# Kernel optimization log

Hardware: AMD Instinct MI355X
Metric: run time of the kernel (lower is better)

## Reference

```python
import jax, jax.numpy as jnp
import numpy as np

N_NODES = 500_000
N_EDGES = 8_000_000
NUM_GRAPHS = 512


def _glorot(key, shape):
    lim = float(np.sqrt(6.0 / (shape[0] + shape[1])))
    return jax.random.uniform(key, shape, jnp.float32, -lim, lim)


def setup_inputs() -> dict:
    key = jax.random.key(0)
    ks = jax.random.split(key, 10)
    x = jax.random.normal(ks[0], (N_NODES, 3), jnp.float32)
    edge_index = jax.random.randint(ks[1], (2, N_EDGES), 0, N_NODES, jnp.int64)
    batch = jnp.sort(jax.random.randint(ks[2], (N_NODES,), 0, NUM_GRAPHS, jnp.int64))
    return {
        "x": x,
        "edge_index": edge_index,
        "batch": batch,
        # GCNConv weights stored [in, out]; bias [out]
        "W1": _glorot(ks[3], (3, 16)),
        "b1": jnp.zeros((16,), jnp.float32),
        "W2": _glorot(ks[4], (16, 32)),
        "b2": jnp.zeros((32,), jnp.float32),
        "fW1": _glorot(ks[5], (32, 64)),
        "fb1": jnp.zeros((64,), jnp.float32),
        "fW2": _glorot(ks[6], (64, 3)),
        "fb2": jnp.zeros((3,), jnp.float32),
    }


def _gcn_conv(x, edge_index, W, b):
    n = x.shape[0]
    src, dst = edge_index[0], edge_index[1]
    h = x @ W  # [N, out]
    ones = jnp.ones((edge_index.shape[1],), h.dtype)
    deg = jax.ops.segment_sum(ones, dst, num_segments=n) + 1.0  # in-degree + self loop
    dinv = jax.lax.rsqrt(deg)
    norm = dinv[src] * dinv[dst]  # [E]
    agg = jax.ops.segment_sum(norm[:, None] * h[src], dst, num_segments=n)
    # self-loop contribution: norm_ii = dinv_i^2
    return agg + (dinv * dinv)[:, None] * h + b


def reference(x, edge_index, batch, W1, b1, W2, b2, fW1, fb1, fW2, fb2):
    h = jax.nn.relu(_gcn_conv(x, edge_index, W1, b1))
    h = jax.nn.relu(_gcn_conv(h, edge_index, W2, b2))
    # global_mean_pool over graph ids
    sums = jax.ops.segment_sum(h, batch, num_segments=NUM_GRAPHS)
    cnts = jax.ops.segment_sum(jnp.ones((h.shape[0],), h.dtype), batch, num_segments=NUM_GRAPHS)
    pooled = sums / jnp.maximum(cnts, 1.0)[:, None]  # [G, 32]
    z = jax.nn.relu(pooled @ fW1 + fb1)
    z = z @ fW2 + fb2
    return jax.nn.log_softmax(z, axis=1)
```

## Files before the change

kernel.cpp:

```cpp
#include <hip/hip_runtime.h>
#include <hip/hip_bf16.h>

constexpr int N_NODES    = 500000;
constexpr int N_EDGES    = 8000000;
constexpr int NUM_GRAPHS = 512;

constexpr int BSHIFT = 11;
constexpr int BSIZE  = 1 << BSHIFT;
constexpr int NBKT   = (N_NODES + BSIZE - 1) / BSIZE;
constexpr int EPB    = 4096;
constexpr int NBLK_A = (N_EDGES + EPB - 1) / EPB;
constexpr int NH     = NBKT * NBLK_A;
constexpr int SCAN_B = 256;
constexpr int NSB    = (NH + SCAN_B - 1) / SCAN_B;
constexpr int TSH    = 16;
constexpr int CAP    = 20480;

__device__ __forceinline__ float bf_lo(unsigned u) { return __uint_as_float(u << 16); }
__device__ __forceinline__ float bf_hi(unsigned u) { return __uint_as_float(u & 0xFFFF0000u); }
__device__ __forceinline__ unsigned short f2bf(float f) {
  unsigned u = __float_as_uint(f);
  return (unsigned short)((u + 0x7FFFu + ((u >> 16) & 1u)) >> 16);
}
__device__ __forceinline__ unsigned packbf(float a, float b) {
  return (unsigned)f2bf(a) | ((unsigned)f2bf(b) << 16);
}

__device__ __forceinline__ unsigned f2e4m3(float x) {
  x = fminf(x, 448.0f);
  unsigned xb = __float_as_uint(x);
  int e = (int)(xb >> 23) - 127;
  if (e < -6) {
    int m = (int)rintf(x * 512.0f);
    return (m <= 7) ? (unsigned)m : 0x08u;
  }
  unsigned lsb = (xb >> 20) & 1;
  unsigned r = xb + 0x7FFFFu + lsb;
  int e2 = (int)(r >> 23) - 127;
  unsigned m3 = (r >> 20) & 7;
  return (unsigned)(((e2 + 7) << 3) | m3);
}
__device__ __forceinline__ float e4m3f(unsigned b) {
  unsigned e = (b >> 3) & 0xF, m = b & 7;
  float norm = __uint_as_float(((e + 120u) << 23) | (m << 20));
  float den = (float)m * 0.001953125f;
  return e ? norm : den;
}

__global__ void k_hist(const int* __restrict__ dst, int* __restrict__ H) {
  __shared__ int h[NBKT];
  for (int i = threadIdx.x; i < NBKT; i += blockDim.x) h[i] = 0;
  __syncthreads();
  int e0 = blockIdx.x * EPB;
  int e1 = min(e0 + EPB, N_EDGES);
  for (int e = e0 + threadIdx.x; e < e1; e += blockDim.x)
    atomicAdd(&h[dst[e] >> BSHIFT], 1);
  __syncthreads();
  for (int i = threadIdx.x; i < NBKT; i += blockDim.x)
    H[i * NBLK_A + blockIdx.x] = h[i];
}

__global__ void k_scan1(const int* __restrict__ in, int* __restrict__ out,
                        int* __restrict__ bsum, int n) {
  __shared__ int tmp[SCAN_B];
  int t = threadIdx.x;
  int i = blockIdx.x * SCAN_B + t;
  int v = (i < n) ? in[i] : 0;
  tmp[t] = v;
  __syncthreads();
  for (int off = 1; off < SCAN_B; off <<= 1) {
    int a = (t >= off) ? tmp[t - off] : 0;
    __syncthreads();
    tmp[t] += a;
    __syncthreads();
  }
  if (i < n) out[i] = tmp[t] - v;
  if (t == SCAN_B - 1) bsum[blockIdx.x] = tmp[t];
}

__global__ void k_scan2(int* __restrict__ bsum, int nb) {
  __shared__ int tmp[SCAN_B];
  int t = threadIdx.x;
  int carry = 0;
  for (int base = 0; base < nb; base += SCAN_B) {
    int i = base + t;
    int v = (i < nb) ? bsum[i] : 0;
    tmp[t] = v;
    __syncthreads();
    for (int off = 1; off < SCAN_B; off <<= 1) {
      int a = (t >= off) ? tmp[t - off] : 0;
      __syncthreads();
      tmp[t] += a;
      __syncthreads();
    }
    if (i < nb) bsum[i] = carry + tmp[t] - v;
    carry += tmp[SCAN_B - 1];
    __syncthreads();
  }
}

__device__ __forceinline__ int s_at(const int* Sarr, const int* bsum, int idx) {
  return Sarr[idx] + bsum[idx >> 8];
}

__global__ void k_scatter_bkt(const int* __restrict__ src, const int* __restrict__ dst,
                              const int* __restrict__ Sarr, const int* __restrict__ bsum,
                              int* __restrict__ pairs) {
  __shared__ int lcnt[256];
  __shared__ int lofs[256];
  __shared__ int base[256];
  __shared__ int pout[EPB];
  __shared__ unsigned char bout[EPB];
  int t = threadIdx.x;
  int blk = blockIdx.x;
  int e0 = blk * EPB;
  int e1 = min(e0 + EPB, N_EDGES);
  int ne = e1 - e0;
  lcnt[t] = 0;
  __syncthreads();
  for (int e = e0 + t; e < e1; e += 256)
    atomicAdd(&lcnt[dst[e] >> BSHIFT], 1);
  __syncthreads();
  lofs[t] = lcnt[t];
  __syncthreads();
  for (int off = 1; off < 256; off <<= 1) {
    int v = (t >= off) ? lofs[t - off] : 0;
    __syncthreads();
    lofs[t] += v;
    __syncthreads();
  }
  lofs[t] -= lcnt[t];
  base[t] = (t < NBKT) ? s_at(Sarr, bsum, t * NBLK_A + blk) : 0;
  lcnt[t] = 0;
  __syncthreads();
  for (int e = e0 + t; e < e1; e += 256) {
    int d = dst[e], s = src[e];
    int b = d >> BSHIFT;
    int r = atomicAdd(&lcnt[b], 1);
    int q = lofs[b] + r;
    pout[q] = ((d & (BSIZE - 1)) << 19) | s;
    bout[q] = (unsigned char)b;
  }
  __syncthreads();
  for (int li = t; li < ne; li += 256) {
    int b = bout[li];
    pairs[base[b] + (li - lofs[b])] = pout[li];
  }
}

__global__ void __launch_bounds__(1024)
k_csr(const int* __restrict__ pairs, const int* __restrict__ Sarr,
      const int* __restrict__ bsum, const float* __restrict__ x,
      int* __restrict__ ssrc, int* __restrict__ offs,
      float* __restrict__ dinv, unsigned* __restrict__ xsb) {
  __shared__ int hist[8192];
  __shared__ int sout[CAP];
  __shared__ int tmp[1024];
  int t = threadIdx.x;
  int bkt = blockIdx.x >> 1;
  int h = blockIdx.x & 1;
  int e0 = s_at(Sarr, bsum, bkt * NBLK_A);
  int e1 = (bkt + 1 < NBKT) ? s_at(Sarr, bsum, (bkt + 1) * NBLK_A) : N_EDGES;
#pragma unroll
  for (int j = 0; j < 8; ++j) hist[t + (j << 10)] = 0;
  __syncthreads();
  int lc = 0;
  for (int e = e0 + t; e < e1; e += 1024) {
    int p = pairs[e];
    int nl = p >> 19;
    int s = p & 0x7FFFF;
    if ((nl >> 10) == h) atomicAdd(&hist[((s >> TSH) << 10) | (nl & 1023)], 1);
    else if ((nl >> 10) == 0) lc++;
  }
  tmp[t] = lc;
  __syncthreads();
  for (int off = 512; off > 0; off >>= 1) {
    if (t < off) tmp[t] += tmp[t + off];
    __syncthreads();
  }
  int halfbase = h ? tmp[0] : 0;
  __syncthreads();
  int c[8];
  int tsum = 0;
#pragma unroll
  for (int j = 0; j < 8; ++j) { c[j] = hist[(j << 10) | t]; tsum += c[j]; }
  tmp[t] = tsum;
  __syncthreads();
  for (int off = 1; off < 1024; off <<= 1) {
    int a = (t >= off) ? tmp[t - off] : 0;
    __syncthreads();
    tmp[t] += a;
    __syncthreads();
  }
  int run = tmp[t] - tsum;
  int total = tmp[1023];
  {
    int b = run;
#pragma unroll
    for (int j = 0; j < 8; ++j) { int cc = c[j]; hist[(j << 10) | t] = b; b += cc; }
  }
  int n = (bkt << BSHIFT) + (h << 10) + t;
  if (n < N_NODES) {
    offs[n] = e0 + halfbase + run;
    float di = rsqrtf((float)tsum + 1.0f);
    dinv[n] = di;
    const float* xs = x + (size_t)n * 3;
    uint2 v = make_uint2(packbf(di * xs[0], di * xs[1]), packbf(di * xs[2], 0.0f));
    *(uint2*)(xsb + (size_t)n * 2) = v;
  }
  __syncthreads();
  int base = e0 + halfbase;
  if (total <= CAP) {
    for (int e = e0 + t; e < e1; e += 1024) {
      int p = pairs[e];
      int nl = p >> 19;
      if ((nl >> 10) != h) continue;
      int s = p & 0x7FFFF;
      int r = atomicAdd(&hist[((s >> TSH) << 10) | (nl & 1023)], 1);
      sout[r] = s;
    }
    __syncthreads();
    for (int q = t; q < total; q += 1024)
      ssrc[base + q] = sout[q];
  } else {
    for (int e = e0 + t; e < e1; e += 1024) {
      int p = pairs[e];
      int nl = p >> 19;
      if ((nl >> 10) != h) continue;
      int s = p & 0x7FFFF;
      int r = atomicAdd(&hist[((s >> TSH) << 10) | (nl & 1023)], 1);
      ssrc[base + r] = s;
    }
  }
  if (bkt == 0 && h == 0 && t == 0) offs[N_NODES] = N_EDGES;
}

__global__ void k_g1f1(const int* __restrict__ ssrc, const int* __restrict__ offs,
                       const unsigned* __restrict__ xsb, const float* __restrict__ dinv,
                       const float* __restrict__ W1, const float* __restrict__ b1,
                       unsigned* __restrict__ ub) {
  unsigned t = blockIdx.x * blockDim.x + threadIdx.x;
  unsigned n = t >> 1;
  int j = t & 1;
  if (n >= (unsigned)N_NODES) return;
  int o0 = offs[n], o1 = offs[n + 1];
  float a0 = 0.0f, a1 = 0.0f;
  int i = o0;
  for (; i + 1 < o1; i += 2) {
    int s0 = ssrc[i], s1 = ssrc[i + 1];
    unsigned q0 = xsb[(size_t)s0 * 2 + j];
    unsigned q1 = xsb[(size_t)s1 * 2 + j];
    a0 += bf_lo(q0) + bf_lo(q1);
    a1 += bf_hi(q0) + bf_hi(q1);
  }
  if (i < o1) {
    unsigned q = xsb[(size_t)ssrc[i] * 2 + j];
    a0 += bf_lo(q); a1 += bf_hi(q);
  }
  float oth0 = __shfl_xor(a0, 1);
  float oth1 = __shfl_xor(a1, 1);
  float A0 = j ? oth0 : a0;
  float A1v = j ? oth1 : a1;
  float A2v = j ? a0 : oth0;
  float di = dinv[n];
  uint2 xq = *(const uint2*)&xsb[(size_t)n * 2];
  float t0 = di * (A0 + bf_lo(xq.x));
  float t1 = di * (A1v + bf_hi(xq.x));
  float t2 = di * (A2v + bf_lo(xq.y));
  unsigned w0 = 0, w1 = 0;
#pragma unroll
  for (int q8 = 0; q8 < 4; ++q8) {
    int f = 8 * j + 2 * q8;
    float v0 = t0 * W1[f]     + t1 * W1[16 + f]     + t2 * W1[32 + f]     + b1[f];
    float v1 = t0 * W1[f + 1] + t1 * W1[16 + f + 1] + t2 * W1[32 + f + 1] + b1[f + 1];
    unsigned pb = f2e4m3(di * fmaxf(v0, 0.0f)) | (f2e4m3(di * fmaxf(v1, 0.0f)) << 8);
    if (q8 < 2) w0 |= pb << (16 * q8); else w1 |= pb << (16 * (q8 - 2));
  }
  *(uint2*)&ub[(size_t)n * 4 + j * 2] = make_uint2(w0, w1);
}

__global__ void k_gather2(const int* __restrict__ ssrc, const int* __restrict__ offs,
                          const unsigned* __restrict__ ub, float* __restrict__ A2) {
  __shared__ float lut[128];
  if (threadIdx.x < 128) lut[threadIdx.x] = e4m3f(threadIdx.x);
  __syncthreads();
  unsigned t = blockIdx.x * blockDim.x + threadIdx.x;
  unsigned n = t >> 2;
  int j = t & 3;
  if (n >= (unsigned)N_NODES) return;
  int o0 = offs[n], o1 = offs[n + 1];
  unsigned qs = ub[(size_t)n * 4 + j];
  float a0 = lut[qs & 0x7F];
  float a1 = lut[(qs >> 8) & 0x7F];
  float a2 = lut[(qs >> 16) & 0x7F];
  float a3 = lut[(qs >> 24) & 0x7F];
  int i = o0;
  for (; i + 1 < o1; i += 2) {
    int s0 = ssrc[i], s1 = ssrc[i + 1];
    unsigned q0 = ub[(size_t)s0 * 4 + j];
    unsigned q1 = ub[(size_t)s1 * 4 + j];
    a0 += lut[q0 & 0x7F]         + lut[q1 & 0x7F];
    a1 += lut[(q0 >> 8) & 0x7F]  + lut[(q1 >> 8) & 0x7F];
    a2 += lut[(q0 >> 16) & 0x7F] + lut[(q1 >> 16) & 0x7F];
    a3 += lut[(q0 >> 24) & 0x7F] + lut[(q1 >> 24) & 0x7F];
  }
  if (i < o1) {
    unsigned q = ub[(size_t)ssrc[i] * 4 + j];
    a0 += lut[q & 0x7F];
    a1 += lut[(q >> 8) & 0x7F];
    a2 += lut[(q >> 16) & 0x7F];
    a3 += lut[(q >> 24) & 0x7F];
  }
  *(float4*)&A2[(size_t)n * 16 + j * 4] = make_float4(a0, a1, a2, a3);
}

__global__ void k_pool2(const float* __restrict__ A2,
                        const float* __restrict__ W2, const float* __restrict__ b2,
                        const float* __restrict__ dinv, const int* __restrict__ batch,
                        float* __restrict__ sums) {
  int f = threadIdx.x & 31, sub = threadIdx.x >> 5;
  int n0 = blockIdx.x * 128 + sub * 16;
  int n1 = min(n0 + 16, N_NODES);
  if (n0 >= n1) return;
  float w2col[16];
#pragma unroll
  for (int k = 0; k < 16; ++k) w2col[k] = W2[k * 32 + f];
  float bf = b2[f];
  int cur = batch[n0];
  float acc = 0.0f;
  for (int n = n0; n < n1; ++n) {
    int g = batch[n];
    if (g != cur) { atomicAdd(&sums[(size_t)cur * 32 + f], acc); acc = 0.0f; cur = g; }
    const float4* a2p = (const float4*)(A2 + (size_t)n * 16);
    float4 aa0 = a2p[0], aa1 = a2p[1], aa2 = a2p[2], aa3 = a2p[3];
    float v = aa0.x * w2col[0]  + aa0.y * w2col[1]  + aa0.z * w2col[2]  + aa0.w * w2col[3]
            + aa1.x * w2col[4]  + aa1.y * w2col[5]  + aa1.z * w2col[6]  + aa1.w * w2col[7]
            + aa2.x * w2col[8]  + aa2.y * w2col[9]  + aa2.z * w2col[10] + aa2.w * w2col[11]
            + aa3.x * w2col[12] + aa3.y * w2col[13] + aa3.z * w2col[14] + aa3.w * w2col[15];
    v = dinv[n] * v + bf;
    acc += fmaxf(v, 0.0f);
  }
  atomicAdd(&sums[(size_t)cur * 32 + f], acc);
}

__global__ void k_mlp(const float* __restrict__ sums, const int* __restrict__ batch,
                      const float* __restrict__ fW1, const float* __restrict__ fb1,
                      const float* __restrict__ fW2, const float* __restrict__ fb2,
                      float* __restrict__ out) {
  __shared__ float w1s[32 * 64];
  __shared__ float w2s[64 * 3];
  __shared__ float b1s[64];
  __shared__ float b2s[3];
  for (int i = threadIdx.x; i < 32 * 64; i += blockDim.x) w1s[i] = fW1[i];
  for (int i = threadIdx.x; i < 64 * 3; i += blockDim.x) w2s[i] = fW2[i];
  for (int i = threadIdx.x; i < 64; i += blockDim.x) b1s[i] = fb1[i];
  for (int i = threadIdx.x; i < 3; i += blockDim.x) b2s[i] = fb2[i];
  __syncthreads();
  int g = blockIdx.x * blockDim.x + threadIdx.x;
  if (g >= NUM_GRAPHS) return;
  int lo = 0, hi = N_NODES;
  while (lo < hi) { int mid = (lo + hi) >> 1; if (batch[mid] < g) lo = mid + 1; else hi = mid; }
  int s0 = lo;
  int lo2 = s0, hi2 = N_NODES;
  while (lo2 < hi2) { int mid = (lo2 + hi2) >> 1; if (batch[mid] < g + 1) lo2 = mid + 1; else hi2 = mid; }
  float c = fmaxf((float)(lo2 - s0), 1.0f);
  float p[32];
#pragma unroll
  for (int i = 0; i < 32; ++i) p[i] = sums[(size_t)g * 32 + i] / c;
  float z2[3] = {b2s[0], b2s[1], b2s[2]};
  for (int j = 0; j < 64; ++j) {
    float a = b1s[j];
#pragma unroll
    for (int i = 0; i < 32; ++i) a += p[i] * w1s[i * 64 + j];
    a = fmaxf(a, 0.0f);
#pragma unroll
    for (int k = 0; k < 3; ++k) z2[k] += a * w2s[j * 3 + k];
  }
  float m = fmaxf(fmaxf(z2[0], z2[1]), z2[2]);
  float l = logf(expf(z2[0] - m) + expf(z2[1] - m) + expf(z2[2] - m));
#pragma unroll
  for (int k = 0; k < 3; ++k) out[(size_t)g * 3 + k] = z2[k] - m - l;
}

extern "C" void kernel_launch(void* const* d_in, const int* in_sizes, int n_in,
                              void* d_out, int out_size, void* d_ws, size_t ws_size,
                              hipStream_t stream) {
  const float* x     = (const float*)d_in[0];
  const int*   ei    = (const int*)d_in[1];
  const int*   batch = (const int*)d_in[2];
  const float* W1    = (const float*)d_in[3];
  const float* b1    = (const float*)d_in[4];
  const float* W2    = (const float*)d_in[5];
  const float* b2    = (const float*)d_in[6];
  const float* fW1   = (const float*)d_in[7];
  const float* fb1   = (const float*)d_in[8];
  const float* fW2   = (const float*)d_in[9];
  const float* fb2   = (const float*)d_in[10];
  const int* src = ei;
  const int* dst = ei + N_EDGES;

  float* ws       = (float*)d_ws;
  float* dinv     = ws;
  unsigned* xsb   = (unsigned*)(dinv + 524288);
  unsigned* ub    = xsb + 1048576;
  float* scratch  = (float*)(ub + 4194304);
  float* sums     = scratch + 2000000;
  int* offs       = (int*)(sums + 16384);
  int* ssrc       = offs + 524288;
  int* pairs      = ssrc + 8000000;
  int* H    = (int*)scratch;
  int* Sarr = H + 478730;
  int* bsum = Sarr + 478730;
  float* A2 = (float*)pairs;

  hipMemsetAsync(sums, 0, (size_t)NUM_GRAPHS * 32 * 4, stream);

  const int B = 256;
  k_hist<<<NBLK_A, B, 0, stream>>>(dst, H);
  k_scan1<<<NSB, SCAN_B, 0, stream>>>(H, Sarr, bsum, NH);
  k_scan2<<<1, SCAN_B, 0, stream>>>(bsum, NSB);
  k_scatter_bkt<<<NBLK_A, B, 0, stream>>>(src, dst, Sarr, bsum, pairs);
  k_csr<<<NBKT * 2, 1024, 0, stream>>>(pairs, Sarr, bsum, x, ssrc, offs, dinv, xsb);
  k_g1f1<<<((size_t)N_NODES * 2 + B - 1) / B, B, 0, stream>>>(ssrc, offs, xsb, dinv, W1, b1, ub);
  k_gather2<<<((size_t)N_NODES * 4 + B - 1) / B, B, 0, stream>>>(ssrc, offs, ub, A2);
  k_pool2<<<(N_NODES + 127) / 128, B, 0, stream>>>(A2, W2, b2, dinv, batch, sums);
  k_mlp<<<(NUM_GRAPHS + B - 1) / B, B, 0, stream>>>(sums, batch, fW1, fb1, fW2, fb2, (float*)d_out);
}
```

Baseline: 365.0 us.

## Split layer-2 gather into two feature halves for smaller working set

```diff
diff --git a/kernel.cpp b/kernel.cpp
--- a/kernel.cpp
+++ b/kernel.cpp
@@ -238,7 +238,7 @@
 __global__ void k_g1f1(const int* __restrict__ ssrc, const int* __restrict__ offs,
                        const unsigned* __restrict__ xsb, const float* __restrict__ dinv,
                        const float* __restrict__ W1, const float* __restrict__ b1,
-                       unsigned* __restrict__ ub) {
+                       unsigned* __restrict__ ub0, unsigned* __restrict__ ub1) {
   unsigned t = blockIdx.x * blockDim.x + threadIdx.x;
   unsigned n = t >> 1;
   int j = t & 1;
@@ -276,20 +276,21 @@
     unsigned pb = f2e4m3(di * fmaxf(v0, 0.0f)) | (f2e4m3(di * fmaxf(v1, 0.0f)) << 8);
     if (q8 < 2) w0 |= pb << (16 * q8); else w1 |= pb << (16 * (q8 - 2));
   }
-  *(uint2*)&ub[(size_t)n * 4 + j * 2] = make_uint2(w0, w1);
-}
-
-__global__ void k_gather2(const int* __restrict__ ssrc, const int* __restrict__ offs,
-                          const unsigned* __restrict__ ub, float* __restrict__ A2) {
+  unsigned* ubt = j ? ub1 : ub0;
+  *(uint2*)&ubt[(size_t)n * 2] = make_uint2(w0, w1);
+}
+
+__global__ void k_gather2h(const int* __restrict__ ssrc, const int* __restrict__ offs,
+                           const unsigned* __restrict__ ubt, float* __restrict__ A2h) {
   __shared__ float lut[128];
   if (threadIdx.x < 128) lut[threadIdx.x] = e4m3f(threadIdx.x);
   __syncthreads();
   unsigned t = blockIdx.x * blockDim.x + threadIdx.x;
-  unsigned n = t >> 2;
-  int j = t & 3;
+  unsigned n = t >> 1;
+  int j = t & 1;
   if (n >= (unsigned)N_NODES) return;
   int o0 = offs[n], o1 = offs[n + 1];
-  unsigned qs = ub[(size_t)n * 4 + j];
+  unsigned qs = ubt[(size_t)n * 2 + j];
   float a0 = lut[qs & 0x7F];
   float a1 = lut[(qs >> 8) & 0x7F];
   float a2 = lut[(qs >> 16) & 0x7F];
@@ -297,24 +298,24 @@
   int i = o0;
   for (; i + 1 < o1; i += 2) {
     int s0 = ssrc[i], s1 = ssrc[i + 1];
-    unsigned q0 = ub[(size_t)s0 * 4 + j];
-    unsigned q1 = ub[(size_t)s1 * 4 + j];
+    unsigned q0 = ubt[(size_t)s0 * 2 + j];
+    unsigned q1 = ubt[(size_t)s1 * 2 + j];
     a0 += lut[q0 & 0x7F]         + lut[q1 & 0x7F];
     a1 += lut[(q0 >> 8) & 0x7F]  + lut[(q1 >> 8) & 0x7F];
     a2 += lut[(q0 >> 16) & 0x7F] + lut[(q1 >> 16) & 0x7F];
     a3 += lut[(q0 >> 24) & 0x7F] + lut[(q1 >> 24) & 0x7F];
   }
   if (i < o1) {
-    unsigned q = ub[(size_t)ssrc[i] * 4 + j];
+    unsigned q = ubt[(size_t)ssrc[i] * 2 + j];
     a0 += lut[q & 0x7F];
     a1 += lut[(q >> 8) & 0x7F];
     a2 += lut[(q >> 16) & 0x7F];
     a3 += lut[(q >> 24) & 0x7F];
   }
-  *(float4*)&A2[(size_t)n * 16 + j * 4] = make_float4(a0, a1, a2, a3);
-}
-
-__global__ void k_pool2(const float* __restrict__ A2,
+  *(float4*)&A2h[(size_t)n * 8 + j * 4] = make_float4(a0, a1, a2, a3);
+}
+
+__global__ void k_pool2(const float* __restrict__ A2a, const float* __restrict__ A2b,
                         const float* __restrict__ W2, const float* __restrict__ b2,
                         const float* __restrict__ dinv, const int* __restrict__ batch,
                         float* __restrict__ sums) {
@@ -331,8 +332,9 @@
   for (int n = n0; n < n1; ++n) {
     int g = batch[n];
     if (g != cur) { atomicAdd(&sums[(size_t)cur * 32 + f], acc); acc = 0.0f; cur = g; }
-    const float4* a2p = (const float4*)(A2 + (size_t)n * 16);
-    float4 aa0 = a2p[0], aa1 = a2p[1], aa2 = a2p[2], aa3 = a2p[3];
+    const float4* pa = (const float4*)(A2a + (size_t)n * 8);
+    const float4* pb = (const float4*)(A2b + (size_t)n * 8);
+    float4 aa0 = pa[0], aa1 = pa[1], aa2 = pb[0], aa3 = pb[1];
     float v = aa0.x * w2col[0]  + aa0.y * w2col[1]  + aa0.z * w2col[2]  + aa0.w * w2col[3]
             + aa1.x * w2col[4]  + aa1.y * w2col[5]  + aa1.z * w2col[6]  + aa1.w * w2col[7]
             + aa2.x * w2col[8]  + aa2.y * w2col[9]  + aa2.z * w2col[10] + aa2.w * w2col[11]
@@ -402,8 +404,9 @@
   float* ws       = (float*)d_ws;
   float* dinv     = ws;
   unsigned* xsb   = (unsigned*)(dinv + 524288);
-  unsigned* ub    = xsb + 1048576;
-  float* scratch  = (float*)(ub + 4194304);
+  unsigned* ub0   = xsb + 1048576;
+  unsigned* ub1   = ub0 + 1048576;
+  float* scratch  = (float*)(xsb + 1048576 + 4194304);
   float* sums     = scratch + 2000000;
   int* offs       = (int*)(sums + 16384);
   int* ssrc       = offs + 524288;
@@ -411,7 +414,8 @@
   int* H    = (int*)scratch;
   int* Sarr = H + 478730;
   int* bsum = Sarr + 478730;
-  float* A2 = (float*)pairs;
+  float* A2a = (float*)pairs;
+  float* A2b = A2a + 4000000;
 
   hipMemsetAsync(sums, 0, (size_t)NUM_GRAPHS * 32 * 4, stream);
 
@@ -421,8 +425,9 @@
   k_scan2<<<1, SCAN_B, 0, stream>>>(bsum, NSB);
   k_scatter_bkt<<<NBLK_A, B, 0, stream>>>(src, dst, Sarr, bsum, pairs);
   k_csr<<<NBKT * 2, 1024, 0, stream>>>(pairs, Sarr, bsum, x, ssrc, offs, dinv, xsb);
-  k_g1f1<<<((size_t)N_NODES * 2 + B - 1) / B, B, 0, stream>>>(ssrc, offs, xsb, dinv, W1, b1, ub);
-  k_gather2<<<((size_t)N_NODES * 4 + B - 1) / B, B, 0, stream>>>(ssrc, offs, ub, A2);
-  k_pool2<<<(N_NODES + 127) / 128, B, 0, stream>>>(A2, W2, b2, dinv, batch, sums);
+  k_g1f1<<<((size_t)N_NODES * 2 + B - 1) / B, B, 0, stream>>>(ssrc, offs, xsb, dinv, W1, b1, ub0, ub1);
+  k_gather2h<<<((size_t)N_NODES * 2 + B - 1) / B, B, 0, stream>>>(ssrc, offs, ub0, A2a);
+  k_gather2h<<<((size_t)N_NODES * 2 + B - 1) / B, B, 0, stream>>>(ssrc, offs, ub1, A2b);
+  k_pool2<<<(N_NODES + 127) / 128, B, 0, stream>>>(A2a, A2b, W2, b2, dinv, batch, sums);
   k_mlp<<<(NUM_GRAPHS + B - 1) / B, B, 0, stream>>>(sums, batch, fW1, fb1, fW2, fb2, (float*)d_out);
 }
```

Result: slower. 412.6 us (+13.0%).
